# Performance work log

Hardware: AMD Instinct MI355X
Metric: run time of the kernel (lower is better)

The kernel has to match this reference:

```python
import jax, jax.numpy as jnp
import numpy as np

B, LENGTH, D, IN = 32, 32, 384, 384
NCELLS = LENGTH * (LENGTH + 1) // 2  # 528

def _offsets():
    off = np.zeros(LENGTH, dtype=np.int64)
    for lvl in range(1, LENGTH):
        off[lvl] = off[lvl - 1] + (LENGTH - (lvl - 1))
    return off

_OFF = _offsets()

def _inside_index(level):
    Ls = LENGTH - level
    pos = np.arange(Ls)[:, None]
    k = np.arange(level)[None, :]
    left = _OFF[k] + pos                      # span (k, pos)
    right = _OFF[level - k - 1] + pos + k + 1  # span (level-k-1, pos+k+1)
    return jnp.asarray(left), jnp.asarray(right)

def _outside_index(level):
    Ls = LENGTH - level
    N = LENGTH - level - 1  # constant #contexts per position
    par = np.zeros((Ls, N), dtype=np.int64)
    sib = np.zeros((Ls, N), dtype=np.int64)
    for pos in range(Ls):
        j = 0
        for s in range(LENGTH - pos - level - 1):  # node is left child
            par[pos, j] = _OFF[level + s + 1] + pos
            sib[pos, j] = _OFF[s] + pos + level + 1
            j += 1
        for s in range(pos):  # node is right child
            par[pos, j] = _OFF[level + s + 1] + pos - s - 1
            sib[pos, j] = _OFF[s] + pos - s - 1
            j += 1
    return jnp.asarray(par), jnp.asarray(sib)

def sigma_h(x):
    return x * jnp.tanh(jnp.sqrt(jax.nn.sigmoid(x)))

def layer_norm(x, g, b, eps=1e-5):
    mu = x.mean(-1, keepdims=True)
    var = ((x - mu) ** 2).mean(-1, keepdims=True)
    return (x - mu) * jax.lax.rsqrt(var + eps) * g + b

def compose(l, r, W0, W1, B0, W2, B1):
    h = sigma_h(l @ W0 + r @ W1 + B0)
    return sigma_h(h @ W2 + B1)

def bilinear(u, v, M):
    return jnp.einsum('blnd,de,blne->bln', u, M, v)[..., None]

def setup_inputs() -> dict:
    key = jax.random.key(0)
    ks = jax.random.split(key, 16)
    sc = 1.0 / np.sqrt(D)
    mk = lambda k, shp: (jax.random.normal(k, shp, dtype=jnp.float32) * sc)
    inp = {
        'x': jax.random.normal(ks[0], (B, LENGTH, IN), dtype=jnp.float32),
        'leaf_W': mk(ks[1], (IN, D)), 'leaf_b': jnp.zeros((D,), jnp.float32),
        'in_ln_g': jnp.ones((D,), jnp.float32), 'in_ln_b': jnp.zeros((D,), jnp.float32),
        'out_ln_g': jnp.ones((D,), jnp.float32), 'out_ln_b': jnp.zeros((D,), jnp.float32),
        'root_h': jax.random.normal(ks[2], (D,), dtype=jnp.float32) * 0.02,
        'in_bi': mk(ks[3], (D, D)), 'out_bi': mk(ks[4], (D, D)),
        'in_W0': mk(ks[5], (D, D)), 'in_W1': mk(ks[6], (D, D)),
        'in_B0': jnp.zeros((D,), jnp.float32),
        'in_W2': mk(ks[7], (D, D)), 'in_B1': jnp.zeros((D,), jnp.float32),
        'out_W0': mk(ks[8], (D, D)), 'out_W1': mk(ks[9], (D, D)),
        'out_B0': jnp.zeros((D,), jnp.float32),
        'out_W2': mk(ks[10], (D, D)), 'out_B1': jnp.zeros((D,), jnp.float32),
    }
    return inp

def reference(x, leaf_W, leaf_b, in_ln_g, in_ln_b, out_ln_g, out_ln_b, root_h,
              in_bi, out_bi, in_W0, in_W1, in_B0, in_W2, in_B1,
              out_W0, out_W1, out_B0, out_W2, out_B1):
    # leaf transform
    h0 = layer_norm(sigma_h(x @ leaf_W + leaf_b), in_ln_g, in_ln_b)
    ih = jnp.zeros((B, NCELLS, D), x.dtype).at[:, :LENGTH].set(h0)
    is_ = jnp.zeros((B, NCELLS, 1), x.dtype)
    # inside pass (CKY chart, level-by-level)
    for level in range(1, LENGTH):
        li, ri = _inside_index(level)
        lh, rh = ih[:, li], ih[:, ri]   # [B, Ls, level, D]
        ls, rs = is_[:, li], is_[:, ri]
        sc = bilinear(lh, rh, in_bi) + ls + rs
        p = jax.nn.softmax(sc, axis=2)
        xc = compose(lh, rh, in_W0, in_W1, in_B0, in_W2, in_B1)
        hbar = layer_norm((p * xc).sum(2), in_ln_g, in_ln_b)
        sbar = (p * sc).sum(2)
        o = int(_OFF[level]); Ls = LENGTH - level
        ih = ih.at[:, o:o + Ls].set(hbar)
        is_ = is_.at[:, o:o + Ls].set(sbar)
    # outside pass
    oh = jnp.zeros((B, NCELLS, D), x.dtype)
    os_ = jnp.zeros((B, NCELLS, 1), x.dtype)
    root = layer_norm(jnp.broadcast_to(root_h, (B, 1, D)), out_ln_g, out_ln_b)
    oh = oh.at[:, -1:].set(root)
    for level in range(LENGTH - 2, -1, -1):
        pi, si = _outside_index(level)
        ph, sh = oh[:, pi], ih[:, si]   # parent outside / sibling inside
        ps, ss = os_[:, pi], is_[:, si]
        sc = bilinear(sh, ph, out_bi) + ss + ps
        p = jax.nn.softmax(sc, axis=2)
        xc = compose(ph, sh, out_W0, out_W1, out_B0, out_W2, out_B1)
        hbar = layer_norm((p * xc).sum(2), out_ln_g, out_ln_b)
        sbar = (p * sc).sum(2)
        o = int(_OFF[level]); Ls = LENGTH - level
        oh = oh.at[:, o:o + Ls].set(hbar)
        os_ = os_.at[:, o:o + Ls].set(sbar)
    return ih, is_, oh, os_
```

## Files before the change

### kernel.cpp

```cpp
#include <hip/hip_runtime.h>
#include <cstddef>

#define BDIM 32
#define LEN 32
#define DD 384
#define NCELLS 528

typedef _Float16 h16;
typedef __attribute__((ext_vector_type(8))) _Float16 v8h;
typedef __attribute__((ext_vector_type(4))) float v4f;

__device__ __forceinline__ int offf(int k) { return k * 32 - ((k * (k - 1)) >> 1); }
static inline int offh(int k) { return k * 32 - ((k * (k - 1)) >> 1); }

__device__ __forceinline__ float sigma_h_f(float x) {
  float s = 1.0f / (1.0f + __expf(-x));
  float r = sqrtf(s);
  float e2 = __expf(2.0f * r);
  float th = 1.0f - 2.0f / (e2 + 1.0f);
  return x * th;
}

__device__ __forceinline__ size_t rowbase(int r, int gLs, int gOff) {
  if (gLs == 0) return (size_t)r;
  int b = r / gLs;
  int p = r - b * gLs;
  return (size_t)b * NCELLS + gOff + p;
}

__device__ __forceinline__ void split16(float v, h16& h, h16& l) {
  h = (h16)v;
  l = (h16)(v - (float)h);
}

__global__ __launch_bounds__(256) void pack3_k(
    const float* __restrict__ w0, const float* __restrict__ w1,
    const float* __restrict__ bi, const float* __restrict__ ow1,
    const float* __restrict__ obi, const float* __restrict__ w2,
    const float* __restrict__ ow2, const float* __restrict__ ow0,
    const float* __restrict__ lw, const float* __restrict__ x,
    h16* __restrict__ WCth, h16* __restrict__ WCtl,
    h16* __restrict__ W2th, h16* __restrict__ W2tl,
    h16* __restrict__ OW2th, h16* __restrict__ OW2tl,
    h16* __restrict__ OW0th, h16* __restrict__ OW0tl,
    h16* __restrict__ LWth, h16* __restrict__ LWtl,
    h16* __restrict__ xh, h16* __restrict__ xl,
    float* __restrict__ isp, float* __restrict__ osp) {
  int i = blockIdx.x * 256 + threadIdx.x;
  if (i < 1920 * 384) {
    int n = i / 384, k = i - n * 384;
    int sel = n / 384, c = n - sel * 384;
    const float* src = sel == 0 ? w0 : sel == 1 ? w1 : sel == 2 ? bi
                       : sel == 3 ? ow1 : obi;
    float v = src[k * 384 + c];
    h16 h, l; split16(v, h, l);
    WCth[i] = h; WCtl[i] = l;
  }
  if (i < 384 * 384) {
    int n = i / 384, k = i - n * 384;
    h16 h, l;
    split16(w2[k * 384 + n], h, l);  W2th[i] = h;  W2tl[i] = l;
    split16(ow2[k * 384 + n], h, l); OW2th[i] = h; OW2tl[i] = l;
    split16(ow0[k * 384 + n], h, l); OW0th[i] = h; OW0tl[i] = l;
    split16(lw[k * 384 + n], h, l);  LWth[i] = h;  LWtl[i] = l;
  }
  if (i < 1024 * 384) {
    h16 h, l; split16(x[i], h, l);
    xh[i] = h; xl[i] = l;
  }
  if (i < BDIM * NCELLS) { isp[i] = 0.0f; osp[i] = 0.0f; }
}

__global__ __launch_bounds__(256) void gemmh(
    const h16* __restrict__ Ahp, const h16* __restrict__ Alp,
    const h16* __restrict__ Bth, const h16* __restrict__ Btl,
    const float* __restrict__ bias, float* __restrict__ C,
    int M, int N, int act, int gLs, int gOff) {
  __shared__ h16 Ah[64][40], Al[64][40];
  __shared__ h16 Bh[128][40], Bl[128][40];
  int tid = threadIdx.x;
  int w = tid >> 6, lane = tid & 63;

  int nbx = gridDim.x, nby = gridDim.y;
  int total = nbx * nby;
  int lin = blockIdx.y * nbx + blockIdx.x;
  int xcd = lin & 7, slot = lin >> 3;
  int qd = total >> 3, rd = total & 7;
  int wk = (xcd < rd ? xcd * (qd + 1) : rd * (qd + 1) + (xcd - rd) * qd) + slot;
  int bx = wk / nby;
  int by = wk - bx * nby;
  int m0 = bx * 64, n0 = by * 128;
  int r = lane & 15, q = lane >> 4;

  v4f acc[4][2];
#pragma unroll
  for (int i = 0; i < 4; ++i)
#pragma unroll
    for (int j = 0; j < 2; ++j) acc[i][j] = (v4f){0.f, 0.f, 0.f, 0.f};

  int sar = tid >> 2;
  int sak = (tid & 3) << 3;
  const h16* Aph = nullptr;
  const h16* Apl = nullptr;
  if (m0 + sar < M) {
    size_t rb = (size_t)(m0 + sar) * DD;
    Aph = Ahp + rb + sak;
    Apl = Alp + rb + sak;
  }
  int sbc = tid >> 1;
  int sbk = (tid & 1) << 4;
  const h16* Bph = Bth + (size_t)(n0 + sbc) * DD + sbk;
  const h16* Bpl = Btl + (size_t)(n0 + sbc) * DD + sbk;

  for (int k0 = 0; k0 < DD; k0 += 32) {
    v8h a_h = (v8h){0.f, 0.f, 0.f, 0.f, 0.f, 0.f, 0.f, 0.f};
    v8h a_l = a_h;
    if (Aph) {
      a_h = *reinterpret_cast<const v8h*>(Aph + k0);
      a_l = *reinterpret_cast<const v8h*>(Apl + k0);
    }
    v8h b_h0 = *reinterpret_cast<const v8h*>(Bph + k0);
    v8h b_h1 = *reinterpret_cast<const v8h*>(Bph + k0 + 8);
    v8h b_l0 = *reinterpret_cast<const v8h*>(Bpl + k0);
    v8h b_l1 = *reinterpret_cast<const v8h*>(Bpl + k0 + 8);
    __syncthreads();
    *reinterpret_cast<v8h*>(&Ah[sar][sak]) = a_h;
    *reinterpret_cast<v8h*>(&Al[sar][sak]) = a_l;
    *reinterpret_cast<v8h*>(&Bh[sbc][sbk]) = b_h0;
    *reinterpret_cast<v8h*>(&Bh[sbc][sbk + 8]) = b_h1;
    *reinterpret_cast<v8h*>(&Bl[sbc][sbk]) = b_l0;
    *reinterpret_cast<v8h*>(&Bl[sbc][sbk + 8]) = b_l1;
    __syncthreads();
    v8h afh[4], afl[4], bfh[2], bfl[2];
#pragma unroll
    for (int i = 0; i < 4; ++i) {
      afh[i] = *reinterpret_cast<const v8h*>(&Ah[i * 16 + r][q * 8]);
      afl[i] = *reinterpret_cast<const v8h*>(&Al[i * 16 + r][q * 8]);
    }
#pragma unroll
    for (int j = 0; j < 2; ++j) {
      bfh[j] = *reinterpret_cast<const v8h*>(&Bh[w * 32 + j * 16 + r][q * 8]);
      bfl[j] = *reinterpret_cast<const v8h*>(&Bl[w * 32 + j * 16 + r][q * 8]);
    }
#pragma unroll
    for (int i = 0; i < 4; ++i)
#pragma unroll
      for (int j = 0; j < 2; ++j) {
        acc[i][j] = __builtin_amdgcn_mfma_f32_16x16x32_f16(afl[i], bfh[j], acc[i][j], 0, 0, 0);
        acc[i][j] = __builtin_amdgcn_mfma_f32_16x16x32_f16(afh[i], bfl[j], acc[i][j], 0, 0, 0);
        acc[i][j] = __builtin_amdgcn_mfma_f32_16x16x32_f16(afh[i], bfh[j], acc[i][j], 0, 0, 0);
      }
  }

#pragma unroll
  for (int i = 0; i < 4; ++i) {
#pragma unroll
    for (int reg = 0; reg < 4; ++reg) {
      int rr = m0 + i * 16 + q * 4 + reg;
      if (rr >= M) continue;
      size_t cb = rowbase(rr, gLs, gOff) * (size_t)N;
#pragma unroll
      for (int j = 0; j < 2; ++j) {
        int col = n0 + w * 32 + j * 16 + r;
        float v = acc[i][j][reg];
        if (bias) v += bias[col];
        if (act) v = sigma_h_f(v);
        C[cb + col] = v;
      }
    }
  }
}

__global__ __launch_bounds__(256) void k1s(
    const float* __restrict__ PC, const float* __restrict__ P0,
    const float* __restrict__ vArr, float* __restrict__ scores,
    h16* __restrict__ Hh, h16* __restrict__ Hl,
    const float* __restrict__ B0, int lvl, int np, int Ls, int inside) {
  int g = blockIdx.x;
  int b = g / Ls, pos = g - b * Ls;
  int tid = threadIdx.x, lane = tid & 63, wv = tid >> 6;
  __shared__ float b0s[384];
  size_t cb = (size_t)b * NCELLS;
  for (int k = tid; k < 384; k += 256) b0s[k] = B0[k];
  __syncthreads();
  int n = blockIdx.y * 4 + wv;
  if (n >= np) return;

  const float *u, *v, *A0r, *A1r;
  if (inside) {
    int lc = offf(n) + pos;
    int rc = offf(np - 1 - n) + pos + n + 1;
    u   = PC + (cb + lc) * 1920 + 768;
    v   = vArr + (cb + rc) * (size_t)DD;
    A0r = PC + (cb + lc) * 1920;
    A1r = PC + (cb + rc) * 1920 + 384;
  } else {
    int par, sib;
    int cnt0 = 31 - pos - lvl;
    if (n < cnt0) { par = offf(lvl + n + 1) + pos; sib = offf(n) + pos + lvl + 1; }
    else { int s2 = n - cnt0; par = offf(lvl + s2 + 1) + pos - s2 - 1; sib = offf(s2) + pos - s2 - 1; }
    u   = PC + (cb + sib) * 1920 + 1536;
    v   = vArr + (cb + par) * (size_t)DD;
    A0r = P0 + (cb + par) * (size_t)DD;
    A1r = PC + (cb + sib) * 1920 + 1152;
  }
  float s = 0.0f;
#pragma unroll
  for (int jj = 0; jj < 6; ++jj) s += u[lane + 64 * jj] * v[lane + 64 * jj];
#pragma unroll
  for (int o = 32; o; o >>= 1) s += __shfl_xor(s, o, 64);
  if (lane == 0) scores[(size_t)g * np + n] = s;
  size_t hb = ((size_t)g * np + n) * DD;
#pragma unroll
  for (int jj = 0; jj < 6; ++jj) {
    int k = lane + 64 * jj;
    float hv = sigma_h_f(A0r[k] + A1r[k] + b0s[k]);
    h16 h = (h16)hv;
    Hh[hb + k] = h;
    Hl[hb + k] = (h16)(hv - (float)h);
  }
}

__global__ __launch_bounds__(256) void k3_sm(
    const float* __restrict__ XC, const float* __restrict__ scores,
    const float* __restrict__ isp, float* __restrict__ sOut,
    const float* __restrict__ lng, const float* __restrict__ lnb,
    float* __restrict__ outArr, h16* __restrict__ outh, h16* __restrict__ outl,
    int lvl, int np, int Ls, int offL, int inside, int doSM) {
  int g = blockIdx.x;
  int b = g / Ls, pos = g - b * Ls;
  int tid = threadIdx.x, lane = tid & 63, wv = tid >> 6;
  __shared__ float pb[32];
  __shared__ float comb[384];
  __shared__ float r1[2], r2[2];
  size_t cb = (size_t)b * NCELLS;

  if (doSM) {
    if (wv == 0) {
      float sc = -3.0e38f;
      if (lane < np) {
        float biasv;
        if (inside) {
          int lc = offf(lane) + pos;
          int rc = offf(np - 1 - lane) + pos + lane + 1;
          biasv = isp[cb + lc] + isp[cb + rc];
        } else {
          int par, sib;
          int cnt0 = 31 - pos - lvl;
          if (lane < cnt0) { par = offf(lvl + lane + 1) + pos; sib = offf(lane) + pos + lvl + 1; }
          else { int s2 = lane - cnt0; par = offf(lvl + s2 + 1) + pos - s2 - 1; sib = offf(s2) + pos - s2 - 1; }
          biasv = isp[cb + sib] + sOut[cb + par];
        }
        sc = scores[(size_t)g * np + lane] + biasv;
      }
      float m = sc;
#pragma unroll
      for (int o = 32; o; o >>= 1) m = fmaxf(m, __shfl_xor(m, o, 64));
      float e = (lane < np) ? __expf(sc - m) : 0.0f;
      float S = e;
#pragma unroll
      for (int o = 32; o; o >>= 1) S += __shfl_xor(S, o, 64);
      float pn = e / S;
      if (lane < np) pb[lane] = pn;
      float sb = (lane < np) ? pn * sc : 0.0f;
#pragma unroll
      for (int o = 32; o; o >>= 1) sb += __shfl_xor(sb, o, 64);
      if (lane == 0) sOut[cb + offL + pos] = sb;
    }
  } else {
    if (tid == 0) pb[0] = 1.0f;
  }
  __syncthreads();

  int gi = tid >> 7, t2 = tid & 127;
  float a0 = 0.f, a1 = 0.f, a2 = 0.f;
  const float* base = XC + (size_t)g * np * DD;
  for (int n = gi; n < np; n += 2) {
    float pw = pb[n];
    const float* row = base + (size_t)n * DD;
    a0 += pw * row[t2];
    a1 += pw * row[t2 + 128];
    a2 += pw * row[t2 + 256];
  }
  if (gi == 1) { comb[t2] = a0; comb[t2 + 128] = a1; comb[t2 + 256] = a2; }
  __syncthreads();
  if (gi == 0) { a0 += comb[t2]; a1 += comb[t2 + 128]; a2 += comb[t2 + 256]; }
  float s = a0 + a1 + a2;
#pragma unroll
  for (int o = 32; o; o >>= 1) s += __shfl_xor(s, o, 64);
  if (gi == 0 && lane == 0) r1[wv] = s;
  __syncthreads();
  float mean = (r1[0] + r1[1]) * (1.0f / 384.0f);
  float d0 = a0 - mean, d1 = a1 - mean, d2 = a2 - mean;
  float q = d0 * d0 + d1 * d1 + d2 * d2;
#pragma unroll
  for (int o = 32; o; o >>= 1) q += __shfl_xor(q, o, 64);
  if (gi == 0 && lane == 0) r2[wv] = q;
  __syncthreads();
  if (gi == 0) {
    float var = (r2[0] + r2[1]) * (1.0f / 384.0f);
    float inv = rsqrtf(var + 1e-5f);
    size_t ob = ((size_t)b * NCELLS + offL + pos) * DD;
    float* out = outArr + ob;
    float v0 = d0 * inv * lng[t2]       + lnb[t2];
    float v1 = d1 * inv * lng[t2 + 128] + lnb[t2 + 128];
    float v2 = d2 * inv * lng[t2 + 256] + lnb[t2 + 256];
    out[t2]       = v0;
    out[t2 + 128] = v1;
    out[t2 + 256] = v2;
    size_t sb = (size_t)g * DD;
    h16 h;
    h = (h16)v0; outh[sb + t2]       = h; outl[sb + t2]       = (h16)(v0 - (float)h);
    h = (h16)v1; outh[sb + t2 + 128] = h; outl[sb + t2 + 128] = (h16)(v1 - (float)h);
    h = (h16)v2; outh[sb + t2 + 256] = h; outl[sb + t2 + 256] = (h16)(v2 - (float)h);
  }
}

__global__ __launch_bounds__(384) void root_k(
    const float* __restrict__ rooth, const float* __restrict__ lng,
    const float* __restrict__ lnb, const float* __restrict__ W0,
    float* __restrict__ ohp, float* __restrict__ P0) {
  int tid = threadIdx.x;
  int lane = tid & 63, wv = tid >> 6;
  __shared__ float rl[384];
  __shared__ float r1[6], r2[6];
  float x = rooth[tid];
  float s = x;
#pragma unroll
  for (int o = 32; o; o >>= 1) s += __shfl_xor(s, o, 64);
  if (lane == 0) r1[wv] = s;
  __syncthreads();
  float mean = (r1[0] + r1[1] + r1[2] + r1[3] + r1[4] + r1[5]) * (1.0f / 384.0f);
  float d = x - mean;
  float q = d * d;
#pragma unroll
  for (int o = 32; o; o >>= 1) q += __shfl_xor(q, o, 64);
  if (lane == 0) r2[wv] = q;
  __syncthreads();
  float var = (r2[0] + r2[1] + r2[2] + r2[3] + r2[4] + r2[5]) * (1.0f / 384.0f);
  float inv = rsqrtf(var + 1e-5f);
  float v = d * inv * lng[tid] + lnb[tid];
  rl[tid] = v;
  __syncthreads();
  for (int b2 = 0; b2 < BDIM; ++b2)
    ohp[((size_t)b2 * NCELLS + 527) * DD + tid] = v;
  float acc = 0.0f;
  for (int d2 = 0; d2 < 384; ++d2) acc += rl[d2] * W0[(size_t)d2 * 384 + tid];
  for (int b2 = 0; b2 < BDIM; ++b2)
    P0[((size_t)b2 * NCELLS + 527) * DD + tid] = acc;
}

extern "C" void kernel_launch(void* const* d_in, const int* in_sizes, int n_in,
                              void* d_out, int out_size, void* d_ws, size_t ws_size,
                              hipStream_t stream) {
  const float* x        = (const float*)d_in[0];
  const float* leaf_W   = (const float*)d_in[1];
  const float* leaf_b   = (const float*)d_in[2];
  const float* in_ln_g  = (const float*)d_in[3];
  const float* in_ln_b  = (const float*)d_in[4];
  const float* out_ln_g = (const float*)d_in[5];
  const float* out_ln_b = (const float*)d_in[6];
  const float* root_h   = (const float*)d_in[7];
  const float* in_bi    = (const float*)d_in[8];
  const float* out_bi   = (const float*)d_in[9];
  const float* in_W0    = (const float*)d_in[10];
  const float* in_W1    = (const float*)d_in[11];
  const float* in_B0    = (const float*)d_in[12];
  const float* in_W2    = (const float*)d_in[13];
  const float* in_B1    = (const float*)d_in[14];
  const float* out_W0   = (const float*)d_in[15];
  const float* out_W1   = (const float*)d_in[16];
  const float* out_B0   = (const float*)d_in[17];
  const float* out_W2   = (const float*)d_in[18];
  const float* out_B1   = (const float*)d_in[19];

  float* ih  = (float*)d_out;
  float* isp = ih + (size_t)BDIM * NCELLS * DD;
  float* oh  = isp + (size_t)BDIM * NCELLS;
  float* osp = oh + (size_t)BDIM * NCELLS * DD;

  float* PC  = (float*)d_ws;
  float* P0  = PC + (size_t)32440320;
  float* XCb = P0 + (size_t)6488064;
  float* Pw  = XCb + (size_t)12189696;
  h16* Hh    = (h16*)(Pw + 31744);
  h16* Hl    = Hh + (size_t)12189696;
  h16* WCth  = Hl + (size_t)12189696;
  h16* WCtl  = WCth + (size_t)737280;
  h16* W2th  = WCtl + (size_t)737280;
  h16* W2tl  = W2th + (size_t)147456;
  h16* OW2th = W2tl + (size_t)147456;
  h16* OW2tl = OW2th + (size_t)147456;
  h16* OW0th = OW2tl + (size_t)147456;
  h16* OW0tl = OW0th + (size_t)147456;
  h16* LWth  = OW0tl + (size_t)147456;
  h16* LWtl  = LWth + (size_t)147456;
  h16* xh = Hh;
  h16* xl = Hl;
  h16* Ch = Hh + (size_t)16384 * DD;
  h16* Cl = Hl + (size_t)16384 * DD;

  pack3_k<<<2880, 256, 0, stream>>>(in_W0, in_W1, in_bi, out_W1, out_bi,
                                    in_W2, out_W2, out_W0, leaf_W, x,
                                    WCth, WCtl, W2th, W2tl, OW2th, OW2tl,
                                    OW0th, OW0tl, LWth, LWtl, xh, xl,
                                    isp, osp);

  gemmh<<<dim3(16, 3), 256, 0, stream>>>(xh, xl, LWth, LWtl, leaf_b, XCb, 1024, 384, 1, 0, 0);
  k3_sm<<<1024, 256, 0, stream>>>(XCb, Pw, isp, isp, in_ln_g, in_ln_b,
                                  ih, Ch, Cl, 0, 1, 32, 0, 1, 0);
  gemmh<<<dim3(16, 15), 256, 0, stream>>>(Ch, Cl, WCth, WCtl, nullptr, PC, 1024, 1920, 0, 32, 0);

  for (int L = 1; L < LEN; ++L) {
    int Ls = LEN - L, G = BDIM * Ls, M = G * L, off = offh(L);
    k1s<<<dim3(G, (L + 3) / 4), 256, 0, stream>>>(PC, nullptr, ih, Pw, Hh, Hl,
                                                  in_B0, L, L, Ls, 1);
    gemmh<<<dim3((M + 63) / 64, 3), 256, 0, stream>>>(Hh, Hl, W2th, W2tl, in_B1, XCb, M, 384, 1, 0, 0);
    k3_sm<<<G, 256, 0, stream>>>(XCb, Pw, isp, isp, in_ln_g, in_ln_b,
                                 ih, Ch, Cl, L, L, Ls, off, 1, 1);
    gemmh<<<dim3((G + 63) / 64, 15), 256, 0, stream>>>(Ch, Cl, WCth, WCtl, nullptr, PC, G, 1920, 0, Ls, off);
  }

  root_k<<<1, 384, 0, stream>>>(root_h, out_ln_g, out_ln_b, out_W0, oh, P0);

  for (int L = LEN - 2; L >= 0; --L) {
    int Ls = LEN - L, G = BDIM * Ls, Nc = LEN - 1 - L, M = G * Nc, off = offh(L);
    k1s<<<dim3(G, (Nc + 3) / 4), 256, 0, stream>>>(PC, P0, oh, Pw, Hh, Hl,
                                                   out_B0, L, Nc, Ls, 0);
    gemmh<<<dim3((M + 63) / 64, 3), 256, 0, stream>>>(Hh, Hl, OW2th, OW2tl, out_B1, XCb, M, 384, 1, 0, 0);
    k3_sm<<<G, 256, 0, stream>>>(XCb, Pw, isp, osp, out_ln_g, out_ln_b,
                                 oh, Ch, Cl, L, Nc, Ls, off, 0, 1);
    gemmh<<<dim3((G + 63) / 64, 3), 256, 0, stream>>>(Ch, Cl, OW0th, OW0tl, nullptr, P0, G, 384, 0, Ls, off);
  }
}
```

Before: 4.135 ms.

## Fuse first compose layer into second-layer GEMM A-tile load

```diff
diff --git a/kernel.cpp b/kernel.cpp
--- a/kernel.cpp
+++ b/kernel.cpp
@@ -171,38 +171,161 @@
   }
 }
 
-__global__ __launch_bounds__(256) void k1s(
+__global__ __launch_bounds__(256) void gemmf(
+    const float* __restrict__ PC, const float* __restrict__ P0,
+    const h16* __restrict__ Bth, const h16* __restrict__ Btl,
+    const float* __restrict__ B0, const float* __restrict__ B1,
+    float* __restrict__ C, int M, int np, int lvl, int Ls, int inside) {
+  __shared__ h16 Ah[64][40], Al[64][40];
+  __shared__ h16 Bh[128][40], Bl[128][40];
+  int tid = threadIdx.x;
+  int w = tid >> 6, lane = tid & 63;
+
+  int nbx = gridDim.x, nby = gridDim.y;
+  int total = nbx * nby;
+  int lin = blockIdx.y * nbx + blockIdx.x;
+  int xcd = lin & 7, slot = lin >> 3;
+  int qd = total >> 3, rd = total & 7;
+  int wk = (xcd < rd ? xcd * (qd + 1) : rd * (qd + 1) + (xcd - rd) * qd) + slot;
+  int bx = wk / nby;
+  int by = wk - bx * nby;
+  int m0 = bx * 64, n0 = by * 128;
+  int r = lane & 15, q = lane >> 4;
+
+  v4f acc[4][2];
+#pragma unroll
+  for (int i = 0; i < 4; ++i)
+#pragma unroll
+    for (int j = 0; j < 2; ++j) acc[i][j] = (v4f){0.f, 0.f, 0.f, 0.f};
+
+  int sar = tid >> 2;
+  int sak = (tid & 3) << 3;
+  const float* A0r = nullptr;
+  const float* A1r = nullptr;
+  {
+    int row = m0 + sar;
+    if (row < M) {
+      int g = row / np, n = row - g * np;
+      int b = g / Ls, pos = g - b * Ls;
+      size_t cb = (size_t)b * NCELLS;
+      if (inside) {
+        int lc = offf(n) + pos;
+        int rc = offf(np - 1 - n) + pos + n + 1;
+        A0r = PC + (cb + lc) * 1920 + sak;
+        A1r = PC + (cb + rc) * 1920 + 384 + sak;
+      } else {
+        int par, sib;
+        int cnt0 = 31 - pos - lvl;
+        if (n < cnt0) { par = offf(lvl + n + 1) + pos; sib = offf(n) + pos + lvl + 1; }
+        else { int s2 = n - cnt0; par = offf(lvl + s2 + 1) + pos - s2 - 1; sib = offf(s2) + pos - s2 - 1; }
+        A0r = P0 + (cb + par) * (size_t)DD + sak;
+        A1r = PC + (cb + sib) * 1920 + 1152 + sak;
+      }
+    }
+  }
+  int sbc = tid >> 1;
+  int sbk = (tid & 1) << 4;
+  const h16* Bph = Bth + (size_t)(n0 + sbc) * DD + sbk;
+  const h16* Bpl = Btl + (size_t)(n0 + sbc) * DD + sbk;
+
+  for (int k0 = 0; k0 < DD; k0 += 32) {
+    float4 x0, x1, y0, y1;
+    if (A0r) {
+      x0 = *reinterpret_cast<const float4*>(A0r + k0);
+      x1 = *reinterpret_cast<const float4*>(A0r + k0 + 4);
+      y0 = *reinterpret_cast<const float4*>(A1r + k0);
+      y1 = *reinterpret_cast<const float4*>(A1r + k0 + 4);
+    }
+    float4 c0 = *reinterpret_cast<const float4*>(B0 + k0 + sak);
+    float4 c1 = *reinterpret_cast<const float4*>(B0 + k0 + sak + 4);
+    v8h b_h0 = *reinterpret_cast<const v8h*>(Bph + k0);
+    v8h b_h1 = *reinterpret_cast<const v8h*>(Bph + k0 + 8);
+    v8h b_l0 = *reinterpret_cast<const v8h*>(Bpl + k0);
+    v8h b_l1 = *reinterpret_cast<const v8h*>(Bpl + k0 + 8);
+    __syncthreads();
+    {
+      v8h hi = (v8h){0.f, 0.f, 0.f, 0.f, 0.f, 0.f, 0.f, 0.f}, lo = hi;
+      if (A0r) {
+        float av[8] = {x0.x, x0.y, x0.z, x0.w, x1.x, x1.y, x1.z, x1.w};
+        float bv[8] = {y0.x, y0.y, y0.z, y0.w, y1.x, y1.y, y1.z, y1.w};
+        float cv[8] = {c0.x, c0.y, c0.z, c0.w, c1.x, c1.y, c1.z, c1.w};
+#pragma unroll
+        for (int t = 0; t < 8; ++t) {
+          float hv = sigma_h_f(av[t] + bv[t] + cv[t]);
+          h16 h = (h16)hv;
+          hi[t] = h;
+          lo[t] = (h16)(hv - (float)h);
+        }
+      }
+      *reinterpret_cast<v8h*>(&Ah[sar][sak]) = hi;
+      *reinterpret_cast<v8h*>(&Al[sar][sak]) = lo;
+    }
+    *reinterpret_cast<v8h*>(&Bh[sbc][sbk]) = b_h0;
+    *reinterpret_cast<v8h*>(&Bh[sbc][sbk + 8]) = b_h1;
+    *reinterpret_cast<v8h*>(&Bl[sbc][sbk]) = b_l0;
+    *reinterpret_cast<v8h*>(&Bl[sbc][sbk + 8]) = b_l1;
+    __syncthreads();
+    v8h afh[4], afl[4], bfh[2], bfl[2];
+#pragma unroll
+    for (int i = 0; i < 4; ++i) {
+      afh[i] = *reinterpret_cast<const v8h*>(&Ah[i * 16 + r][q * 8]);
+      afl[i] = *reinterpret_cast<const v8h*>(&Al[i * 16 + r][q * 8]);
+    }
+#pragma unroll
+    for (int j = 0; j < 2; ++j) {
+      bfh[j] = *reinterpret_cast<const v8h*>(&Bh[w * 32 + j * 16 + r][q * 8]);
+      bfl[j] = *reinterpret_cast<const v8h*>(&Bl[w * 32 + j * 16 + r][q * 8]);
+    }
+#pragma unroll
+    for (int i = 0; i < 4; ++i)
+#pragma unroll
+      for (int j = 0; j < 2; ++j) {
+        acc[i][j] = __builtin_amdgcn_mfma_f32_16x16x32_f16(afl[i], bfh[j], acc[i][j], 0, 0, 0);
+        acc[i][j] = __builtin_amdgcn_mfma_f32_16x16x32_f16(afh[i], bfl[j], acc[i][j], 0, 0, 0);
+        acc[i][j] = __builtin_amdgcn_mfma_f32_16x16x32_f16(afh[i], bfh[j], acc[i][j], 0, 0, 0);
+      }
+  }
+
+#pragma unroll
+  for (int i = 0; i < 4; ++i) {
+#pragma unroll
+    for (int reg = 0; reg < 4; ++reg) {
+      int rr = m0 + i * 16 + q * 4 + reg;
+      if (rr >= M) continue;
+      size_t cb = (size_t)rr * DD;
+#pragma unroll
+      for (int j = 0; j < 2; ++j) {
+        int col = n0 + w * 32 + j * 16 + r;
+        C[cb + col] = sigma_h_f(acc[i][j][reg] + B1[col]);
+      }
+    }
+  }
+}
+
+__global__ __launch_bounds__(256) void k1sc(
     const float* __restrict__ PC, const float* __restrict__ P0,
     const float* __restrict__ vArr, float* __restrict__ scores,
-    h16* __restrict__ Hh, h16* __restrict__ Hl,
-    const float* __restrict__ B0, int lvl, int np, int Ls, int inside) {
+    int lvl, int np, int Ls, int inside) {
   int g = blockIdx.x;
   int b = g / Ls, pos = g - b * Ls;
   int tid = threadIdx.x, lane = tid & 63, wv = tid >> 6;
-  __shared__ float b0s[384];
   size_t cb = (size_t)b * NCELLS;
-  for (int k = tid; k < 384; k += 256) b0s[k] = B0[k];
-  __syncthreads();
   int n = blockIdx.y * 4 + wv;
   if (n >= np) return;
 
-  const float *u, *v, *A0r, *A1r;
+  const float *u, *v;
   if (inside) {
     int lc = offf(n) + pos;
     int rc = offf(np - 1 - n) + pos + n + 1;
-    u   = PC + (cb + lc) * 1920 + 768;
-    v   = vArr + (cb + rc) * (size_t)DD;
-    A0r = PC + (cb + lc) * 1920;
-    A1r = PC + (cb + rc) * 1920 + 384;
+    u = PC + (cb + lc) * 1920 + 768;
+    v = vArr + (cb + rc) * (size_t)DD;
   } else {
     int par, sib;
     int cnt0 = 31 - pos - lvl;
     if (n < cnt0) { par = offf(lvl + n + 1) + pos; sib = offf(n) + pos + lvl + 1; }
     else { int s2 = n - cnt0; par = offf(lvl + s2 + 1) + pos - s2 - 1; sib = offf(s2) + pos - s2 - 1; }
-    u   = PC + (cb + sib) * 1920 + 1536;
-    v   = vArr + (cb + par) * (size_t)DD;
-    A0r = P0 + (cb + par) * (size_t)DD;
-    A1r = PC + (cb + sib) * 1920 + 1152;
+    u = PC + (cb + sib) * 1920 + 1536;
+    v = vArr + (cb + par) * (size_t)DD;
   }
   float s = 0.0f;
 #pragma unroll
@@ -210,15 +333,6 @@
 #pragma unroll
   for (int o = 32; o; o >>= 1) s += __shfl_xor(s, o, 64);
   if (lane == 0) scores[(size_t)g * np + n] = s;
-  size_t hb = ((size_t)g * np + n) * DD;
-#pragma unroll
-  for (int jj = 0; jj < 6; ++jj) {
-    int k = lane + 64 * jj;
-    float hv = sigma_h_f(A0r[k] + A1r[k] + b0s[k]);
-    h16 h = (h16)hv;
-    Hh[hb + k] = h;
-    Hl[hb + k] = (h16)(hv - (float)h);
-  }
 }
 
 __global__ __launch_bounds__(256) void k3_sm(
@@ -413,9 +527,9 @@
 
   for (int L = 1; L < LEN; ++L) {
     int Ls = LEN - L, G = BDIM * Ls, M = G * L, off = offh(L);
-    k1s<<<dim3(G, (L + 3) / 4), 256, 0, stream>>>(PC, nullptr, ih, Pw, Hh, Hl,
-                                                  in_B0, L, L, Ls, 1);
-    gemmh<<<dim3((M + 63) / 64, 3), 256, 0, stream>>>(Hh, Hl, W2th, W2tl, in_B1, XCb, M, 384, 1, 0, 0);
+    k1sc<<<dim3(G, (L + 3) / 4), 256, 0, stream>>>(PC, nullptr, ih, Pw, L, L, Ls, 1);
+    gemmf<<<dim3((M + 63) / 64, 3), 256, 0, stream>>>(PC, nullptr, W2th, W2tl,
+                                                      in_B0, in_B1, XCb, M, L, L, Ls, 1);
     k3_sm<<<G, 256, 0, stream>>>(XCb, Pw, isp, isp, in_ln_g, in_ln_b,
                                  ih, Ch, Cl, L, L, Ls, off, 1, 1);
     gemmh<<<dim3((G + 63) / 64, 15), 256, 0, stream>>>(Ch, Cl, WCth, WCtl, nullptr, PC, G, 1920, 0, Ls, off);
@@ -425,11 +539,12 @@
 
   for (int L = LEN - 2; L >= 0; --L) {
     int Ls = LEN - L, G = BDIM * Ls, Nc = LEN - 1 - L, M = G * Nc, off = offh(L);
-    k1s<<<dim3(G, (Nc + 3) / 4), 256, 0, stream>>>(PC, P0, oh, Pw, Hh, Hl,
-                                                   out_B0, L, Nc, Ls, 0);
-    gemmh<<<dim3((M + 63) / 64, 3), 256, 0, stream>>>(Hh, Hl, OW2th, OW2tl, out_B1, XCb, M, 384, 1, 0, 0);
+    k1sc<<<dim3(G, (Nc + 3) / 4), 256, 0, stream>>>(PC, P0, oh, Pw, L, Nc, Ls, 0);
+    gemmf<<<dim3((M + 63) / 64, 3), 256, 0, stream>>>(PC, P0, OW2th, OW2tl,
+                                                      out_B0, out_B1, XCb, M, Nc, L, Ls, 0);
     k3_sm<<<G, 256, 0, stream>>>(XCb, Pw, isp, osp, out_ln_g, out_ln_b,
                                  oh, Ch, Cl, L, Nc, Ls, off, 0, 1);
-    gemmh<<<dim3((G + 63) / 64, 3), 256, 0, stream>>>(Ch, Cl, OW0th, OW0tl, nullptr, P0, G, 384, 0, Ls, off);
-  }
-}
+    if (L > 0)
+      gemmh<<<dim3((G + 63) / 64, 3), 256, 0, stream>>>(Ch, Cl, OW0th, OW0tl, nullptr, P0, G, 384, 0, Ls, off);
+  }
+}
```

New measurement: 4.698 ms. +13.6%, slower.
